# Optimization experiments

Measured on AMD Instinct MI355X. Metric: run time of the kernel, lower is better.

The kernel has to match this reference:

```python
import jax, jax.numpy as jnp
import numpy as np

B = 1      # batch
D = 64     # octree grid side at this level
N = 65536  # active voxels
C = 32     # channels (nin == nout for resblock)
K = 3      # kernel size


def _offsets():
    r = jnp.arange(K) - K // 2
    oz, oy, ox = jnp.meshgrid(r, r, r, indexing='ij')
    return jnp.stack([oz.ravel(), oy.ravel(), ox.ravel()], axis=-1)  # [27,3] (kz,ky,kx order)


def octree_conv3d(values, indices, mask_values, kernel, bias, activation=None):
    # values: [N,Cin], indices: [N,4] (b,z,y,x), mask_values: [N,1]
    Cin = values.shape[-1]
    Cout = kernel.shape[-1]
    taps = kernel.reshape(K * K * K, Cin, Cout)            # kz,ky,kx order == kernel[kz,ky,kx]
    vals = jnp.einsum('nc,tcd->tnd', values, taps)         # [27,N,Cout]
    offs = _offsets()                                      # [27,3]
    coords = indices[:, 1:]                                # [N,3]
    # shift = [0, kz-1, ky-1, kx-1]; clamp to [0, D-1] (stride=inv_stride=1)
    sh = jnp.clip(coords[None, :, :] + offs[:, None, :], 0, D - 1)  # [27,N,3]
    lin = indices[:, 0][None, :] * (D * D * D) + sh[..., 0] * (D * D) + sh[..., 1] * D + sh[..., 2]
    grid = jnp.zeros((B * D * D * D, Cout), dtype=values.dtype)
    grid = grid.at[lin.reshape(-1)].add(vals.reshape(-1, Cout))     # scatter-add == coalesce sum
    out_lin = indices[:, 0] * (D * D * D) + coords[:, 0] * (D * D) + coords[:, 1] * D + coords[:, 2]
    gathered = grid[out_lin]                               # [N,Cout] values at mask positions
    out = (gathered + mask_values * bias[None, :]) * mask_values     # result + mask*bias; result*mask
    if activation is not None:
        out = activation(out)
    return out


def setup_inputs() -> dict:
    key = jax.random.key(0)
    k1, k2, k3, k4, k5, k6 = jax.random.split(key, 6)
    G = B * D * D * D
    perm = jax.random.permutation(k1, G)[:N]               # unique (coalesced) voxel indices
    b = perm // (D * D * D)
    rem = perm % (D * D * D)
    z = rem // (D * D)
    y = (rem // D) % D
    x = rem % D
    indices = jnp.stack([b, z, y, x], axis=-1).astype(jnp.int64)   # [N,4]
    values = jax.random.normal(k2, (N, C), dtype=jnp.float32)
    mask_values = jnp.ones((N, 1), dtype=jnp.float32)
    stdv = 1.0 / np.sqrt(K * K * K * C)
    kern1 = (jax.random.uniform(k3, (K, K, K, C, C)) - 0.5) * 2.0 * stdv
    bias1 = (jax.random.uniform(k4, (C,)) - 0.5) * 2.0 * stdv
    kern2 = (jax.random.uniform(k5, (K, K, K, C, C)) - 0.5) * 2.0 * stdv
    bias2 = (jax.random.uniform(k6, (C,)) - 0.5) * 2.0 * stdv
    return {'values': values, 'indices': indices, 'mask_values': mask_values,
            'kern1': kern1, 'bias1': bias1, 'kern2': kern2, 'bias2': bias2}


def reference(values, indices, mask_values, kern1, bias1, kern2, bias2):
    # OctreeResblock: conv(relu) -> conv -> residual add, all on the sparse index set
    h = octree_conv3d(values, indices, mask_values, kern1, bias1, activation=jax.nn.relu)
    h = octree_conv3d(h, indices, mask_values, kern2, bias2, activation=None)
    return values + h
```

## Files before the change

### kernel.cpp

```cpp
#include <hip/hip_runtime.h>

#define NPTS 65536
#define CCH  32
#define DDIM 64
#define GVOX (DDIM*DDIM*DDIM)
#define MAXTILES 4128
#define NSLOT (MAXTILES*16)

typedef _Float16 half8  __attribute__((ext_vector_type(8)));
typedef _Float16 half4v __attribute__((ext_vector_type(4)));
typedef float    floatx4 __attribute__((ext_vector_type(4)));

__global__ __launch_bounds__(256) void k_prep0(
    int* __restrict__ map, int* __restrict__ sorted, int* __restrict__ pcs,
    const float* __restrict__ values, _Float16* __restrict__ valsh,
    const float* __restrict__ k1, const float* __restrict__ k2,
    _Float16* __restrict__ w1, _Float16* __restrict__ w2,
    _Float16* __restrict__ hh, int* __restrict__ pcoord,
    int* __restrict__ cnt, int* __restrict__ slot)
{
  int tid = blockIdx.x * 256 + threadIdx.x;
  if (tid < GVOX/4) { ((int4*)map)[tid] = make_int4(-1,-1,-1,-1); return; }
  tid -= GVOX/4;
  if (tid < NSLOT) { sorted[tid] = NPTS; return; }
  tid -= NSLOT;
  if (tid < NSLOT) { pcs[tid] = 0; return; }
  tid -= NSLOT;
  if (tid < (NPTS*CCH)/4) {
    float4 v = ((const float4*)values)[tid];
    half4v h = { (_Float16)v.x, (_Float16)v.y, (_Float16)v.z, (_Float16)v.w };
    ((half4v*)valsh)[tid] = h; return;
  }
  tid -= (NPTS*CCH)/4;
  if (tid < 27*CCH*CCH) {
    int t = tid/(CCH*CCH), r = tid%(CCH*CCH);
    int cin = r/CCH, cout = r%CCH;
    int h = cout >> 4, mm = cout & 15, q = cin >> 3, i = cin & 7;
    int o = t*1024 + h*512 + (q*16 + mm)*8 + i;
    w1[o] = (_Float16)k1[tid]; w2[o] = (_Float16)k2[tid]; return;
  }
  tid -= 27*CCH*CCH;
  if (tid < CCH) { valsh[NPTS*CCH+tid] = (_Float16)0.f; hh[NPTS*CCH+tid] = (_Float16)0.f; return; }
  tid -= CCH;
  if (tid < 27) { cnt[tid] = 0; slot[tid] = 0; return; }
  tid -= 27;
  if (tid == 0) pcoord[NPTS] = 0;
}
#define PREP0_THREADS (GVOX/4 + NSLOT + NSLOT + (NPTS*CCH)/4 + 27*CCH*CCH + CCH + 27 + 1)

__global__ __launch_bounds__(256) void k_prep1(const int* __restrict__ idx,
                                               int* __restrict__ map,
                                               int* __restrict__ pcoord,
                                               int* __restrict__ cls,
                                               int* __restrict__ cnt)
{
  __shared__ int lcnt[27];
  if (threadIdx.x < 27) lcnt[threadIdx.x] = 0;
  __syncthreads();
  const int n = blockIdx.x*256 + threadIdx.x;
  const int4 v = ((const int4*)idx)[n];
  const int b = v.x, z = v.y, y = v.z, x = v.w;
  map[((b*DDIM + z)*DDIM + y)*DDIM + x] = n;
  pcoord[n] = (b<<18) | (z<<12) | (y<<6) | x;
  const int cz = (z==0)?0:((z==DDIM-1)?2:1);
  const int cy = (y==0)?0:((y==DDIM-1)?2:1);
  const int cx = (x==0)?0:((x==DDIM-1)?2:1);
  const int c = cz*9 + cy*3 + cx;
  cls[n] = c;
  atomicAdd(&lcnt[c], 1);
  __syncthreads();
  if (threadIdx.x < 27 && lcnt[threadIdx.x]) atomicAdd(&cnt[threadIdx.x], lcnt[threadIdx.x]);
}

__global__ __launch_bounds__(256) void k_prep3(const int* __restrict__ cls,
                                               const int* __restrict__ cnt,
                                               int* __restrict__ slot,
                                               const int* __restrict__ pcoord,
                                               int* __restrict__ sorted,
                                               int* __restrict__ pcs,
                                               int* __restrict__ tileclass,
                                               int* __restrict__ ntiles)
{
  __shared__ int s_clsbase[27];
  __shared__ int s_tstart[28];
  if (threadIdx.x == 0) {
    int b = 0, tb = 0;
#pragma unroll
    for (int c = 0; c < 27; ++c) {
      s_clsbase[c] = b; s_tstart[c] = tb;
      const int ntc = (cnt[c] + 15) >> 4;
      b += ntc << 4; tb += ntc;
    }
    s_tstart[27] = tb;
    if (blockIdx.x == 0) *ntiles = tb;
  }
  __syncthreads();

  if (blockIdx.x < NPTS/256) {
    __shared__ int lcnt[27], lbase[27];
    if (threadIdx.x < 27) lcnt[threadIdx.x] = 0;
    __syncthreads();
    const int n = blockIdx.x*256 + threadIdx.x;
    const int c = cls[n];
    const int lrank = atomicAdd(&lcnt[c], 1);
    __syncthreads();
    if (threadIdx.x < 27)
      lbase[threadIdx.x] = lcnt[threadIdx.x] ? atomicAdd(&slot[threadIdx.x], lcnt[threadIdx.x]) : 0;
    __syncthreads();
    const int s = s_clsbase[c] + lbase[c] + lrank;
    sorted[s] = n;
    pcs[s] = pcoord[n];
  } else {
    const int i = (blockIdx.x - NPTS/256)*256 + threadIdx.x;
    if (i >= MAXTILES) return;
    const int nt = s_tstart[27];
    int c = 13;
    if (i < nt) {
      for (int cc = 0; cc < 27; ++cc)
        if (i >= s_tstart[cc] && i < s_tstart[cc+1]) { c = cc; break; }
    }
    tileclass[i] = c;
  }
}

__global__ __launch_bounds__(256) void k_nbr(const int* __restrict__ pcs,
                                             const int* __restrict__ map,
                                             int* __restrict__ nbr)
{
  const int tid = blockIdx.x*256 + threadIdx.x;
  if (tid >= MAXTILES*432) return;
  const int tile = tid/432, rem = tid%432;
  const int j = rem >> 4, m = rem & 15;
  const int pc = pcs[tile*16 + m];
  const int bb = pc>>18, z = (pc>>12)&63, y = (pc>>6)&63, x = pc&63;
  const int jz = j/9, jy = (j/3)%3, jx = j%3;
  const int nz = min(max(z + jz - 1, 0), DDIM-1);
  const int ny = min(max(y + jy - 1, 0), DDIM-1);
  const int nx = min(max(x + jx - 1, 0), DDIM-1);
  const int s = map[(bb<<18) | (nz<<12) | (ny<<6) | nx];
  nbr[tid] = ((s < 0) ? NPTS : s) * CCH;
}

template<int MODE>
__global__ __launch_bounds__(512, 4) void conv_mfma(
    const _Float16* __restrict__ A,
    const int* __restrict__ nbr,
    const int* __restrict__ sorted,
    const int* __restrict__ tileclass,
    const int* __restrict__ ntp,
    const _Float16* __restrict__ WT,
    const float* __restrict__ bias,
    const float* __restrict__ mask,
    const float* __restrict__ resid,
    _Float16* __restrict__ hout,
    float* __restrict__ fout)
{
  __shared__ _Float16 lw[27*CCH*CCH];
  for (int i = threadIdx.x; i < 3456; i += 512)
    ((half8*)lw)[i] = ((const half8*)WT)[i];
  __syncthreads();

  const int wv   = threadIdx.x >> 6;
  const int tile = blockIdx.x*8 + wv;
  const int lane = threadIdx.x & 63;
  const int m = lane & 15, quad = lane >> 4;
  if (tile >= *ntp) return;

  const int scls = __builtin_amdgcn_readfirstlane(tileclass[tile]);
  const int cz = scls/9, cy = (scls/3)%3, cx = scls%3;

  const int tb = tile*432;
  int srcs[27];
#pragma unroll
  for (int j = 0; j < 27; ++j) srcs[j] = nbr[tb + j*16 + m];

  floatx4 acc0 = {0.f,0.f,0.f,0.f};
  floatx4 acc1 = {0.f,0.f,0.f,0.f};

#pragma unroll
  for (int g = 0; g < 3; ++g) {
    half8 av[9];
#pragma unroll
    for (int u = 0; u < 9; ++u)
      av[u] = *(const half8*)(A + srcs[g*9 + u] + quad*8);
#pragma unroll
    for (int u = 0; u < 9; ++u) {
      const int j = g*9 + u;
      const int jz = j/9, jy = (j/3)%3, jx = j%3;
      const int tz = (cz==1) ? (2-jz) : ((jz==1) ? 1 : ((cz==0) ? 0 : 2));
      const int ty = (cy==1) ? (2-jy) : ((jy==1) ? 1 : ((cy==0) ? 0 : 2));
      const int tx = (cx==1) ? (2-jx) : ((jx==1) ? 1 : ((cx==0) ? 0 : 2));
      const int t  = tz*9 + ty*3 + tx;
      const _Float16* wr = lw + t*1024;
      half8 b0 = *(const half8*)(wr + lane*8);
      half8 b1 = *(const half8*)(wr + 512 + lane*8);
      acc0 = __builtin_amdgcn_mfma_f32_16x16x32_f16(av[u], b0, acc0, 0, 0, 0);
      acc1 = __builtin_amdgcn_mfma_f32_16x16x32_f16(av[u], b1, acc1, 0, 0, 0);
    }
  }

  const float bi0 = bias[m], bi1 = bias[m+16];
#pragma unroll
  for (int reg = 0; reg < 4; ++reg) {
    const int r  = quad*4 + reg;
    const int pr = sorted[tile*16 + r];
    if (pr >= NPTS) continue;
    const float mk = mask[pr];
    float v0 = (acc0[reg] + mk*bi0) * mk;
    float v1 = (acc1[reg] + mk*bi1) * mk;
    if (MODE == 0) {
      v0 = fmaxf(v0, 0.f); v1 = fmaxf(v1, 0.f);
      hout[pr*CCH + m]      = (_Float16)v0;
      hout[pr*CCH + m + 16] = (_Float16)v1;
    } else {
      fout[pr*CCH + m]      = resid[pr*CCH + m]      + v0;
      fout[pr*CCH + m + 16] = resid[pr*CCH + m + 16] + v1;
    }
  }
}


extern "C" void kernel_launch(void* const* d_in, const int* in_sizes, int n_in,
                              void* d_out, int out_size, void* d_ws, size_t ws_size,
                              hipStream_t stream) {
  const float* values = (const float*)d_in[0];
  const int*   indices= (const int*)  d_in[1];
  const float* maskv  = (const float*)d_in[2];
  const float* kern1  = (const float*)d_in[3];
  const float* bias1  = (const float*)d_in[4];
  const float* kern2  = (const float*)d_in[5];
  const float* bias2  = (const float*)d_in[6];
  float* out = (float*)d_out;

  char* ws = (char*)d_ws;
  size_t off = 0;
  auto alloc = [&](size_t bytes) { void* p = ws + off; off = (off + bytes + 255) & ~(size_t)255; return p; };
  int*      map      = (int*)     alloc(GVOX*4);
  int*      pcoord   = (int*)     alloc((NPTS+1)*4);
  int*      cls      = (int*)     alloc(NPTS*4);
  int*      sorted   = (int*)     alloc(NSLOT*4);
  int*      pcs      = (int*)     alloc(NSLOT*4);
  int*      tileclass= (int*)     alloc(MAXTILES*4);
  int*      nbr      = (int*)     alloc((size_t)MAXTILES*432*4);
  int*      cnt      = (int*)     alloc(27*4);
  int*      slot     = (int*)     alloc(27*4);
  int*      ntiles   = (int*)     alloc(4);
  _Float16* valsh    = (_Float16*)alloc((NPTS+1)*CCH*2);
  _Float16* hh       = (_Float16*)alloc((NPTS+1)*CCH*2);
  _Float16* wt1      = (_Float16*)alloc(27*CCH*CCH*2);
  _Float16* wt2      = (_Float16*)alloc(27*CCH*CCH*2);

  k_prep0<<<(PREP0_THREADS + 255)/256, 256, 0, stream>>>(
      map, sorted, pcs, values, valsh, kern1, kern2, wt1, wt2, hh, pcoord, cnt, slot);
  k_prep1<<<NPTS/256, 256, 0, stream>>>(indices, map, pcoord, cls, cnt);
  k_prep3<<<NPTS/256 + (MAXTILES+255)/256, 256, 0, stream>>>(
      cls, cnt, slot, pcoord, sorted, pcs, tileclass, ntiles);
  k_nbr<<<(MAXTILES*432 + 255)/256, 256, 0, stream>>>(pcs, map, nbr);

  conv_mfma<0><<<(MAXTILES + 7)/8, 512, 0, stream>>>(valsh, nbr, sorted, tileclass,
                                                     ntiles, wt1, bias1, maskv, nullptr, hh, nullptr);
  conv_mfma<1><<<(MAXTILES + 7)/8, 512, 0, stream>>>(hh, nbr, sorted, tileclass,
                                                     ntiles, wt2, bias2, maskv, values, nullptr, out);
}
```

Baseline: 128.6 us.

## Fuse all prep and conv kernels into one persistent kernel with grid barriers

Replaces six separate launches with a single persistent 256-block kernel that runs the prep phases and both convolutions, separated by atomic-counter grid barriers. The neighbour table is no longer stored; each wave computes neighbour indices inline from the voxel map. Tile class is derived from shared tile-start offsets instead of a separate array. This removes launch gaps and the nbr array traffic, but relies on all 256 blocks of 1024 threads being co-resident, and the barrier spin has a guard that could silently break correctness if that does not hold.

```diff
diff --git a/kernel.cpp b/kernel.cpp
--- a/kernel.cpp
+++ b/kernel.cpp
@@ -6,217 +6,213 @@
 #define GVOX (DDIM*DDIM*DDIM)
 #define MAXTILES 4128
 #define NSLOT (MAXTILES*16)
+#define NTHREADS 1024
+#define NBLOCKS  256
+#define TTOT (NTHREADS*NBLOCKS)
 
 typedef _Float16 half8  __attribute__((ext_vector_type(8)));
 typedef _Float16 half4v __attribute__((ext_vector_type(4)));
 typedef float    floatx4 __attribute__((ext_vector_type(4)));
 
-__global__ __launch_bounds__(256) void k_prep0(
+#define P0N (GVOX/4 + NSLOT/4 + NSLOT/4 + (NPTS*CCH)/4 + 27*CCH*CCH + CCH + 27)
+
+struct SharedC {
+  _Float16 lw[27*CCH*CCH];
+  int tstart[28];
+  int clsbase[27];
+  int lcnt[27];
+  int lbase[27];
+};
+
+__device__ __forceinline__ void gbar(int* bar, int target) {
+  __syncthreads();
+  if (threadIdx.x == 0) {
+    __threadfence();
+    atomicAdd(bar, 1);
+    int guard = 1 << 24;
+    while (atomicAdd(bar, 0) < target && --guard)
+      __builtin_amdgcn_s_sleep(1);
+    __threadfence();
+  }
+  __syncthreads();
+}
+
+template<int MODE>
+__device__ void conv_phase(SharedC& sh,
+    const _Float16* __restrict__ A, const int* __restrict__ map,
+    const int* __restrict__ pcs, const int* __restrict__ sorted,
+    const _Float16* __restrict__ WT, const float* __restrict__ bias,
+    const float* __restrict__ mask, const float* __restrict__ resid,
+    _Float16* __restrict__ hout, float* __restrict__ fout)
+{
+  for (int i = threadIdx.x; i < 3456; i += NTHREADS)
+    ((half8*)sh.lw)[i] = ((const half8*)WT)[i];
+  __syncthreads();
+
+  const int wv   = threadIdx.x >> 6;
+  const int lane = threadIdx.x & 63;
+  const int m = lane & 15, quad = lane >> 4;
+  const int nt = sh.tstart[27];
+  const float bi0 = bias[m], bi1 = bias[m+16];
+
+  for (int tile = blockIdx.x*16 + wv; tile < nt; tile += NBLOCKS*16) {
+    int scls = 0;
+    for (int cc = 1; cc < 27; ++cc) if (tile >= sh.tstart[cc]) scls = cc;
+    scls = __builtin_amdgcn_readfirstlane(scls);
+    const int cz = scls/9, cy = (scls/3)%3, cx = scls%3;
+
+    const int pc = pcs[tile*16 + m];
+    const int bb = pc>>18, z = (pc>>12)&63, y = (pc>>6)&63, x = pc&63;
+    const int linb = bb << 18;
+    const int az[3] = { max(z-1,0)<<12, z<<12, min(z+1,DDIM-1)<<12 };
+    const int ay[3] = { max(y-1,0)<<6,  y<<6,  min(y+1,DDIM-1)<<6 };
+    const int ax[3] = { max(x-1,0),     x,     min(x+1,DDIM-1) };
+
+    int srcs[27];
+#pragma unroll
+    for (int j = 0; j < 27; ++j) {
+      const int jz = j/9, jy = (j/3)%3, jx = j%3;
+      const int s = map[linb | az[jz] | ay[jy] | ax[jx]];
+      srcs[j] = ((s < 0) ? NPTS : s) * CCH;
+    }
+
+    floatx4 acc0 = {0.f,0.f,0.f,0.f};
+    floatx4 acc1 = {0.f,0.f,0.f,0.f};
+
+#pragma unroll
+    for (int g = 0; g < 3; ++g) {
+      half8 av[9];
+#pragma unroll
+      for (int u = 0; u < 9; ++u)
+        av[u] = *(const half8*)(A + srcs[g*9 + u] + quad*8);
+      __builtin_amdgcn_s_setprio(1);
+#pragma unroll
+      for (int u = 0; u < 9; ++u) {
+        const int j = g*9 + u;
+        const int jz = j/9, jy = (j/3)%3, jx = j%3;
+        const int tz = (cz==1) ? (2-jz) : ((jz==1) ? 1 : ((cz==0) ? 0 : 2));
+        const int ty = (cy==1) ? (2-jy) : ((jy==1) ? 1 : ((cy==0) ? 0 : 2));
+        const int tx = (cx==1) ? (2-jx) : ((jx==1) ? 1 : ((cx==0) ? 0 : 2));
+        const int t  = tz*9 + ty*3 + tx;
+        const _Float16* wr = sh.lw + t*1024;
+        half8 b0 = *(const half8*)(wr + lane*8);
+        half8 b1 = *(const half8*)(wr + 512 + lane*8);
+        acc0 = __builtin_amdgcn_mfma_f32_16x16x32_f16(av[u], b0, acc0, 0, 0, 0);
+        acc1 = __builtin_amdgcn_mfma_f32_16x16x32_f16(av[u], b1, acc1, 0, 0, 0);
+      }
+      __builtin_amdgcn_s_setprio(0);
+    }
+
+#pragma unroll
+    for (int reg = 0; reg < 4; ++reg) {
+      const int r  = quad*4 + reg;
+      const int pr = sorted[tile*16 + r];
+      if (pr >= NPTS) continue;
+      const float mk = mask[pr];
+      float v0 = (acc0[reg] + mk*bi0) * mk;
+      float v1 = (acc1[reg] + mk*bi1) * mk;
+      if (MODE == 0) {
+        v0 = fmaxf(v0, 0.f); v1 = fmaxf(v1, 0.f);
+        hout[pr*CCH + m]      = (_Float16)v0;
+        hout[pr*CCH + m + 16] = (_Float16)v1;
+      } else {
+        fout[pr*CCH + m]      = resid[pr*CCH + m]      + v0;
+        fout[pr*CCH + m + 16] = resid[pr*CCH + m + 16] + v1;
+      }
+    }
+  }
+}
+
+__global__ __launch_bounds__(1024, 4) void megak(
+    const float* __restrict__ values, const int* __restrict__ idx,
+    const float* __restrict__ maskv,
+    const float* __restrict__ k1, const float* __restrict__ bias1,
+    const float* __restrict__ k2, const float* __restrict__ bias2,
     int* __restrict__ map, int* __restrict__ sorted, int* __restrict__ pcs,
-    const float* __restrict__ values, _Float16* __restrict__ valsh,
-    const float* __restrict__ k1, const float* __restrict__ k2,
-    _Float16* __restrict__ w1, _Float16* __restrict__ w2,
-    _Float16* __restrict__ hh, int* __restrict__ pcoord,
-    int* __restrict__ cnt, int* __restrict__ slot)
+    int* __restrict__ cnt, int* __restrict__ slot,
+    _Float16* __restrict__ valsh, _Float16* __restrict__ hh,
+    _Float16* __restrict__ wt1, _Float16* __restrict__ wt2,
+    float* __restrict__ out, int* bar)
 {
-  int tid = blockIdx.x * 256 + threadIdx.x;
-  if (tid < GVOX/4) { ((int4*)map)[tid] = make_int4(-1,-1,-1,-1); return; }
-  tid -= GVOX/4;
-  if (tid < NSLOT) { sorted[tid] = NPTS; return; }
-  tid -= NSLOT;
-  if (tid < NSLOT) { pcs[tid] = 0; return; }
-  tid -= NSLOT;
-  if (tid < (NPTS*CCH)/4) {
-    float4 v = ((const float4*)values)[tid];
-    half4v h = { (_Float16)v.x, (_Float16)v.y, (_Float16)v.z, (_Float16)v.w };
-    ((half4v*)valsh)[tid] = h; return;
-  }
-  tid -= (NPTS*CCH)/4;
-  if (tid < 27*CCH*CCH) {
-    int t = tid/(CCH*CCH), r = tid%(CCH*CCH);
-    int cin = r/CCH, cout = r%CCH;
-    int h = cout >> 4, mm = cout & 15, q = cin >> 3, i = cin & 7;
-    int o = t*1024 + h*512 + (q*16 + mm)*8 + i;
-    w1[o] = (_Float16)k1[tid]; w2[o] = (_Float16)k2[tid]; return;
-  }
-  tid -= 27*CCH*CCH;
-  if (tid < CCH) { valsh[NPTS*CCH+tid] = (_Float16)0.f; hh[NPTS*CCH+tid] = (_Float16)0.f; return; }
-  tid -= CCH;
-  if (tid < 27) { cnt[tid] = 0; slot[tid] = 0; return; }
-  tid -= 27;
-  if (tid == 0) pcoord[NPTS] = 0;
-}
-#define PREP0_THREADS (GVOX/4 + NSLOT + NSLOT + (NPTS*CCH)/4 + 27*CCH*CCH + CCH + 27 + 1)
-
-__global__ __launch_bounds__(256) void k_prep1(const int* __restrict__ idx,
-                                               int* __restrict__ map,
-                                               int* __restrict__ pcoord,
-                                               int* __restrict__ cls,
-                                               int* __restrict__ cnt)
-{
-  __shared__ int lcnt[27];
-  if (threadIdx.x < 27) lcnt[threadIdx.x] = 0;
-  __syncthreads();
-  const int n = blockIdx.x*256 + threadIdx.x;
-  const int4 v = ((const int4*)idx)[n];
-  const int b = v.x, z = v.y, y = v.z, x = v.w;
-  map[((b*DDIM + z)*DDIM + y)*DDIM + x] = n;
-  pcoord[n] = (b<<18) | (z<<12) | (y<<6) | x;
-  const int cz = (z==0)?0:((z==DDIM-1)?2:1);
-  const int cy = (y==0)?0:((y==DDIM-1)?2:1);
-  const int cx = (x==0)?0:((x==DDIM-1)?2:1);
-  const int c = cz*9 + cy*3 + cx;
-  cls[n] = c;
-  atomicAdd(&lcnt[c], 1);
-  __syncthreads();
-  if (threadIdx.x < 27 && lcnt[threadIdx.x]) atomicAdd(&cnt[threadIdx.x], lcnt[threadIdx.x]);
-}
-
-__global__ __launch_bounds__(256) void k_prep3(const int* __restrict__ cls,
-                                               const int* __restrict__ cnt,
-                                               int* __restrict__ slot,
-                                               const int* __restrict__ pcoord,
-                                               int* __restrict__ sorted,
-                                               int* __restrict__ pcs,
-                                               int* __restrict__ tileclass,
-                                               int* __restrict__ ntiles)
-{
-  __shared__ int s_clsbase[27];
-  __shared__ int s_tstart[28];
+  __shared__ SharedC sh;
+  const int gtid = blockIdx.x*NTHREADS + threadIdx.x;
+
+  for (int t0 = gtid; t0 < P0N; t0 += TTOT) {
+    int tid = t0;
+    if (tid < GVOX/4) { ((int4*)map)[tid] = make_int4(-1,-1,-1,-1); continue; }
+    tid -= GVOX/4;
+    if (tid < NSLOT/4) { ((int4*)sorted)[tid] = make_int4(NPTS,NPTS,NPTS,NPTS); continue; }
+    tid -= NSLOT/4;
+    if (tid < NSLOT/4) { ((int4*)pcs)[tid] = make_int4(0,0,0,0); continue; }
+    tid -= NSLOT/4;
+    if (tid < (NPTS*CCH)/4) {
+      float4 v = ((const float4*)values)[tid];
+      half4v h = { (_Float16)v.x, (_Float16)v.y, (_Float16)v.z, (_Float16)v.w };
+      ((half4v*)valsh)[tid] = h; continue;
+    }
+    tid -= (NPTS*CCH)/4;
+    if (tid < 27*CCH*CCH) {
+      int t = tid/(CCH*CCH), r = tid%(CCH*CCH);
+      int cin = r/CCH, cout = r%CCH;
+      int h = cout >> 4, mm = cout & 15, q = cin >> 3, i = cin & 7;
+      int o = t*1024 + h*512 + (q*16 + mm)*8 + i;
+      wt1[o] = (_Float16)k1[tid]; wt2[o] = (_Float16)k2[tid]; continue;
+    }
+    tid -= 27*CCH*CCH;
+    if (tid < CCH) { valsh[NPTS*CCH+tid] = (_Float16)0.f; hh[NPTS*CCH+tid] = (_Float16)0.f; continue; }
+    tid -= CCH;
+    if (tid < 27) { cnt[tid] = 0; slot[tid] = 0; continue; }
+  }
+  gbar(bar, NBLOCKS);
+
+  if (threadIdx.x < 27) sh.lcnt[threadIdx.x] = 0;
+  __syncthreads();
+  int myc = -1, mypc = 0;
+  if (gtid < NPTS) {
+    const int4 v = ((const int4*)idx)[gtid];
+    const int b = v.x, z = v.y, y = v.z, x = v.w;
+    map[((b*DDIM + z)*DDIM + y)*DDIM + x] = gtid;
+    mypc = (b<<18) | (z<<12) | (y<<6) | x;
+    const int cz = (z==0)?0:((z==DDIM-1)?2:1);
+    const int cy = (y==0)?0:((y==DDIM-1)?2:1);
+    const int cx = (x==0)?0:((x==DDIM-1)?2:1);
+    myc = cz*9 + cy*3 + cx;
+    atomicAdd(&sh.lcnt[myc], 1);
+  }
+  __syncthreads();
+  if (threadIdx.x < 27 && sh.lcnt[threadIdx.x])
+    atomicAdd(&cnt[threadIdx.x], sh.lcnt[threadIdx.x]);
+  gbar(bar, 2*NBLOCKS);
+
   if (threadIdx.x == 0) {
     int b = 0, tb = 0;
-#pragma unroll
     for (int c = 0; c < 27; ++c) {
-      s_clsbase[c] = b; s_tstart[c] = tb;
-      const int ntc = (cnt[c] + 15) >> 4;
+      const int cv = atomicAdd(&cnt[c], 0);
+      sh.clsbase[c] = b; sh.tstart[c] = tb;
+      const int ntc = (cv + 15) >> 4;
       b += ntc << 4; tb += ntc;
     }
-    s_tstart[27] = tb;
-    if (blockIdx.x == 0) *ntiles = tb;
-  }
-  __syncthreads();
-
-  if (blockIdx.x < NPTS/256) {
-    __shared__ int lcnt[27], lbase[27];
-    if (threadIdx.x < 27) lcnt[threadIdx.x] = 0;
-    __syncthreads();
-    const int n = blockIdx.x*256 + threadIdx.x;
-    const int c = cls[n];
-    const int lrank = atomicAdd(&lcnt[c], 1);
-    __syncthreads();
-    if (threadIdx.x < 27)
-      lbase[threadIdx.x] = lcnt[threadIdx.x] ? atomicAdd(&slot[threadIdx.x], lcnt[threadIdx.x]) : 0;
-    __syncthreads();
-    const int s = s_clsbase[c] + lbase[c] + lrank;
-    sorted[s] = n;
-    pcs[s] = pcoord[n];
-  } else {
-    const int i = (blockIdx.x - NPTS/256)*256 + threadIdx.x;
-    if (i >= MAXTILES) return;
-    const int nt = s_tstart[27];
-    int c = 13;
-    if (i < nt) {
-      for (int cc = 0; cc < 27; ++cc)
-        if (i >= s_tstart[cc] && i < s_tstart[cc+1]) { c = cc; break; }
-    }
-    tileclass[i] = c;
-  }
-}
-
-__global__ __launch_bounds__(256) void k_nbr(const int* __restrict__ pcs,
-                                             const int* __restrict__ map,
-                                             int* __restrict__ nbr)
-{
-  const int tid = blockIdx.x*256 + threadIdx.x;
-  if (tid >= MAXTILES*432) return;
-  const int tile = tid/432, rem = tid%432;
-  const int j = rem >> 4, m = rem & 15;
-  const int pc = pcs[tile*16 + m];
-  const int bb = pc>>18, z = (pc>>12)&63, y = (pc>>6)&63, x = pc&63;
-  const int jz = j/9, jy = (j/3)%3, jx = j%3;
-  const int nz = min(max(z + jz - 1, 0), DDIM-1);
-  const int ny = min(max(y + jy - 1, 0), DDIM-1);
-  const int nx = min(max(x + jx - 1, 0), DDIM-1);
-  const int s = map[(bb<<18) | (nz<<12) | (ny<<6) | nx];
-  nbr[tid] = ((s < 0) ? NPTS : s) * CCH;
-}
-
-template<int MODE>
-__global__ __launch_bounds__(512, 4) void conv_mfma(
-    const _Float16* __restrict__ A,
-    const int* __restrict__ nbr,
-    const int* __restrict__ sorted,
-    const int* __restrict__ tileclass,
-    const int* __restrict__ ntp,
-    const _Float16* __restrict__ WT,
-    const float* __restrict__ bias,
-    const float* __restrict__ mask,
-    const float* __restrict__ resid,
-    _Float16* __restrict__ hout,
-    float* __restrict__ fout)
-{
-  __shared__ _Float16 lw[27*CCH*CCH];
-  for (int i = threadIdx.x; i < 3456; i += 512)
-    ((half8*)lw)[i] = ((const half8*)WT)[i];
-  __syncthreads();
-
-  const int wv   = threadIdx.x >> 6;
-  const int tile = blockIdx.x*8 + wv;
-  const int lane = threadIdx.x & 63;
-  const int m = lane & 15, quad = lane >> 4;
-  if (tile >= *ntp) return;
-
-  const int scls = __builtin_amdgcn_readfirstlane(tileclass[tile]);
-  const int cz = scls/9, cy = (scls/3)%3, cx = scls%3;
-
-  const int tb = tile*432;
-  int srcs[27];
-#pragma unroll
-  for (int j = 0; j < 27; ++j) srcs[j] = nbr[tb + j*16 + m];
-
-  floatx4 acc0 = {0.f,0.f,0.f,0.f};
-  floatx4 acc1 = {0.f,0.f,0.f,0.f};
-
-#pragma unroll
-  for (int g = 0; g < 3; ++g) {
-    half8 av[9];
-#pragma unroll
-    for (int u = 0; u < 9; ++u)
-      av[u] = *(const half8*)(A + srcs[g*9 + u] + quad*8);
-#pragma unroll
-    for (int u = 0; u < 9; ++u) {
-      const int j = g*9 + u;
-      const int jz = j/9, jy = (j/3)%3, jx = j%3;
-      const int tz = (cz==1) ? (2-jz) : ((jz==1) ? 1 : ((cz==0) ? 0 : 2));
-      const int ty = (cy==1) ? (2-jy) : ((jy==1) ? 1 : ((cy==0) ? 0 : 2));
-      const int tx = (cx==1) ? (2-jx) : ((jx==1) ? 1 : ((cx==0) ? 0 : 2));
-      const int t  = tz*9 + ty*3 + tx;
-      const _Float16* wr = lw + t*1024;
-      half8 b0 = *(const half8*)(wr + lane*8);
-      half8 b1 = *(const half8*)(wr + 512 + lane*8);
-      acc0 = __builtin_amdgcn_mfma_f32_16x16x32_f16(av[u], b0, acc0, 0, 0, 0);
-      acc1 = __builtin_amdgcn_mfma_f32_16x16x32_f16(av[u], b1, acc1, 0, 0, 0);
-    }
-  }
-
-  const float bi0 = bias[m], bi1 = bias[m+16];
-#pragma unroll
-  for (int reg = 0; reg < 4; ++reg) {
-    const int r  = quad*4 + reg;
-    const int pr = sorted[tile*16 + r];
-    if (pr >= NPTS) continue;
-    const float mk = mask[pr];
-    float v0 = (acc0[reg] + mk*bi0) * mk;
-    float v1 = (acc1[reg] + mk*bi1) * mk;
-    if (MODE == 0) {
-      v0 = fmaxf(v0, 0.f); v1 = fmaxf(v1, 0.f);
-      hout[pr*CCH + m]      = (_Float16)v0;
-      hout[pr*CCH + m + 16] = (_Float16)v1;
-    } else {
-      fout[pr*CCH + m]      = resid[pr*CCH + m]      + v0;
-      fout[pr*CCH + m + 16] = resid[pr*CCH + m + 16] + v1;
-    }
-  }
+    sh.tstart[27] = tb;
+  }
+  if (threadIdx.x < 27) sh.lcnt[threadIdx.x] = 0;
+  __syncthreads();
+  int lrank = 0;
+  if (gtid < NPTS) lrank = atomicAdd(&sh.lcnt[myc], 1);
+  __syncthreads();
+  if (threadIdx.x < 27)
+    sh.lbase[threadIdx.x] = sh.lcnt[threadIdx.x] ? atomicAdd(&slot[threadIdx.x], sh.lcnt[threadIdx.x]) : 0;
+  __syncthreads();
+  if (gtid < NPTS) {
+    const int s = sh.clsbase[myc] + sh.lbase[myc] + lrank;
+    sorted[s] = gtid;
+    pcs[s] = mypc;
+  }
+  gbar(bar, 3*NBLOCKS);
+
+  conv_phase<0>(sh, valsh, map, pcs, sorted, wt1, bias1, maskv, nullptr, hh, nullptr);
+  gbar(bar, 4*NBLOCKS);
+
+  conv_phase<1>(sh, hh, map, pcs, sorted, wt2, bias2, maskv, values, nullptr, out);
 }
 
 
@@ -235,30 +231,19 @@
   char* ws = (char*)d_ws;
   size_t off = 0;
   auto alloc = [&](size_t bytes) { void* p = ws + off; off = (off + bytes + 255) & ~(size_t)255; return p; };
-  int*      map      = (int*)     alloc(GVOX*4);
-  int*      pcoord   = (int*)     alloc((NPTS+1)*4);
-  int*      cls      = (int*)     alloc(NPTS*4);
-  int*      sorted   = (int*)     alloc(NSLOT*4);
-  int*      pcs      = (int*)     alloc(NSLOT*4);
-  int*      tileclass= (int*)     alloc(MAXTILES*4);
-  int*      nbr      = (int*)     alloc((size_t)MAXTILES*432*4);
-  int*      cnt      = (int*)     alloc(27*4);
-  int*      slot     = (int*)     alloc(27*4);
-  int*      ntiles   = (int*)     alloc(4);
-  _Float16* valsh    = (_Float16*)alloc((NPTS+1)*CCH*2);
-  _Float16* hh       = (_Float16*)alloc((NPTS+1)*CCH*2);
-  _Float16* wt1      = (_Float16*)alloc(27*CCH*CCH*2);
-  _Float16* wt2      = (_Float16*)alloc(27*CCH*CCH*2);
-
-  k_prep0<<<(PREP0_THREADS + 255)/256, 256, 0, stream>>>(
-      map, sorted, pcs, values, valsh, kern1, kern2, wt1, wt2, hh, pcoord, cnt, slot);
-  k_prep1<<<NPTS/256, 256, 0, stream>>>(indices, map, pcoord, cls, cnt);
-  k_prep3<<<NPTS/256 + (MAXTILES+255)/256, 256, 0, stream>>>(
-      cls, cnt, slot, pcoord, sorted, pcs, tileclass, ntiles);
-  k_nbr<<<(MAXTILES*432 + 255)/256, 256, 0, stream>>>(pcs, map, nbr);
-
-  conv_mfma<0><<<(MAXTILES + 7)/8, 512, 0, stream>>>(valsh, nbr, sorted, tileclass,
-                                                     ntiles, wt1, bias1, maskv, nullptr, hh, nullptr);
-  conv_mfma<1><<<(MAXTILES + 7)/8, 512, 0, stream>>>(hh, nbr, sorted, tileclass,
-                                                     ntiles, wt2, bias2, maskv, values, nullptr, out);
-}
+  int*      map     = (int*)     alloc(GVOX*4);
+  int*      sorted  = (int*)     alloc(NSLOT*4);
+  int*      pcs     = (int*)     alloc(NSLOT*4);
+  int*      cnt     = (int*)     alloc(27*4);
+  int*      slot    = (int*)     alloc(27*4);
+  int*      bar     = (int*)     alloc(256);
+  _Float16* valsh   = (_Float16*)alloc((NPTS+1)*CCH*2);
+  _Float16* hh      = (_Float16*)alloc((NPTS+1)*CCH*2);
+  _Float16* wt1     = (_Float16*)alloc(27*CCH*CCH*2);
+  _Float16* wt2     = (_Float16*)alloc(27*CCH*CCH*2);
+
+  hipMemsetAsync(bar, 0, 4, stream);
+  megak<<<NBLOCKS, NTHREADS, 0, stream>>>(
+      values, indices, maskv, kern1, bias1, kern2, bias2,
+      map, sorted, pcs, cnt, slot, valsh, hh, wt1, wt2, out, bar);
+}
```

Result: slower. 214.4 us (+66.7%).
